# Performance work log

Hardware: AMD Instinct MI355X
Metric: run time of the kernel (lower is better)

## Reference

```python
import jax, jax.numpy as jnp
import numpy as np

IN_DIM = 512
HID = 256
SAMPLE = 8
TAU = 0.5
LAMBDA = 1.0
NUM_MLP = 3


def l2norm(x, axis=-1, eps=1e-12):
    n = jnp.sqrt(jnp.sum(x * x, axis=axis, keepdims=True))
    return x / jnp.maximum(n, eps)


def graphconv(adj, x, W, b):
    # GraphConv: aggregate then linear transform
    return adj @ (x @ W) + b


def mlp(x, Ws, bs):
    h = x
    for i in range(len(Ws) - 1):
        h = jax.nn.relu(h @ Ws[i] + bs[i])
    return h @ Ws[-1] + bs[-1]


def setup_inputs() -> dict:
    key = jax.random.key(0)
    ks = jax.random.split(key, 24)
    N = 16384
    # sparse-ish row-normalized adjacency surrogate (dense storage)
    a1 = jax.random.uniform(ks[0], (N, N), jnp.float32)
    a1 = (a1 > 0.999).astype(jnp.float32)
    adj1 = a1 / jnp.maximum(a1.sum(1, keepdims=True), 1.0)
    a2 = jax.random.uniform(ks[1], (N, N), jnp.float32)
    a2 = (a2 > 0.999).astype(jnp.float32)
    adj2 = a2 / jnp.maximum(a2.sum(1, keepdims=True), 1.0)
    x1 = jax.random.normal(ks[2], (N, IN_DIM), jnp.float32)
    x2 = jax.random.normal(ks[3], (N, IN_DIM), jnp.float32)
    neighbor_idx = jax.random.randint(ks[4], (N, SAMPLE), 0, N)
    neg_idx = jax.random.randint(ks[5], (N, SAMPLE), 0, N)

    def lin(k, fi, fo):
        k1, k2 = jax.random.split(k)
        s = 1.0 / np.sqrt(fi)
        return (jax.random.uniform(k1, (fi, fo), jnp.float32, -s, s),
                jax.random.uniform(k2, (fo,), jnp.float32, -s, s))

    W1, b1 = lin(ks[6], IN_DIM, HID)
    W2, b2 = lin(ks[7], HID, HID)
    tW1, tb1 = lin(ks[8], IN_DIM, HID)
    tW2, tb2 = lin(ks[9], HID, HID)
    projW, projB, semW, semB = [], [], [], []
    for i in range(NUM_MLP):
        w, b = lin(ks[10 + i], HID, HID)
        projW.append(w); projB.append(b)
        w, b = lin(ks[14 + i], HID, HID)
        semW.append(w); semB.append(b)
    return dict(adj1=adj1, adj2=adj2, x1=x1, x2=x2,
                neighbor_idx=neighbor_idx, neg_idx=neg_idx,
                W1=W1, b1=b1, W2=W2, b2=b2,
                tW1=tW1, tb1=tb1, tW2=tW2, tb2=tb2,
                projW0=projW[0], projB0=projB[0], projW1=projW[1], projB1=projB[1], projW2=projW[2], projB2=projB[2],
                semW0=semW[0], semB0=semB[0], semW1=semW[1], semB1=semB[1], semW2=semW[2], semB2=semB[2])


def contrastive_loss(projected_emd, v_emd, samp_u, samp_neg_v):
    # projected_emd, v_emd: [N,1,D]; samp_u, samp_neg_v: [N,S,D]
    pos = jnp.exp(jnp.einsum('nod,nsd->ns', projected_emd, samp_u) / TAU)  # [N,S]
    neg_sum = jnp.sum(jnp.exp(jnp.einsum('nod,nsd->ns', v_emd, samp_neg_v) / TAU), axis=1)  # [N]
    neg_score = jnp.sum(jnp.log(pos + neg_sum[:, None]), axis=1)  # [N]
    pos_score = jnp.sum(jnp.log(pos), axis=1)
    total = jnp.sum(LAMBDA * neg_score - pos_score)
    return total / samp_u.shape[0] / samp_u.shape[1]


def semi_loss(z1, z2):
    z1n = l2norm(z1); z2n = l2norm(z2)
    refl = jnp.exp((z1n @ z1n.T) / TAU)      # [N,N]
    between = jnp.exp((z1n @ z2n.T) / TAU)   # [N,N]
    return -jnp.log(jnp.diagonal(between) / (refl.sum(1) + between.sum(1) - jnp.diagonal(refl)))


def reference(adj1, adj2, x1, x2, neighbor_idx, neg_idx,
              W1, b1, W2, b2, tW1, tb1, tW2, tb2,
              projW0, projB0, projW1, projB1, projW2, projB2,
              semW0, semB0, semW1, semB1, semW2, semB2):
    pW = [projW0, projW1, projW2]; pB = [projB0, projB1, projB2]
    sW = [semW0, semW1, semW2]; sB = [semB0, semB1, semB2]
    h1 = graphconv(adj1, x1, W1, b1)
    h2 = graphconv(adj1, x2, W1, b1)
    h3 = graphconv(adj2, graphconv(adj2, x1, W1, b1), W2, b2)  # v_emd
    u_emd = l2norm(graphconv(adj2, graphconv(adj2, x1, tW1, tb1), tW2, tb2))
    projected = l2norm(mlp(h3, pW, pB))
    h1_proj = l2norm(mlp(h1, sW, sB))
    h2_proj = l2norm(mlp(h2, sW, sB))

    v_norm = l2norm(h3)
    samp_u = u_emd[neighbor_idx]          # [N,S,D]
    samp_neg_v = v_norm[neg_idx]          # [N,S,D]
    gacl = contrastive_loss(projected[:, None, :], v_norm[:, None, :], samp_u, samp_neg_v)

    l1 = semi_loss(h1_proj, h2_proj)
    l2 = semi_loss(h2_proj, h1_proj)
    sem = jnp.mean((l1 + l2) * 0.5)

    total = gacl + 0.6 * sem
    return total, gacl, sem, h3
```

## Files before the change

### kernel.cpp

```cpp
#include <hip/hip_runtime.h>
#include <hip/hip_bf16.h>

#define NN   16384
#define IND  512
#define HID  256
#define SAMP 8
#define CAP  64

typedef __bf16 bf16;
typedef __bf16 bf16x4 __attribute__((ext_vector_type(4)));
typedef __bf16 bf16x8 __attribute__((ext_vector_type(8)));
typedef float  f32x4  __attribute__((ext_vector_type(4)));

#define LOG2E_2 2.8853900817779268f

#define GLOAD_LDS16(gptr, lptr) \
  __builtin_amdgcn_global_load_lds((const __attribute__((address_space(1))) void*)(gptr), \
                                   (__attribute__((address_space(3))) void*)(lptr), 16, 0, 0)

__global__ void cvt_x(const float* __restrict__ a, bf16* __restrict__ oa,
                      const float* __restrict__ b, bf16* __restrict__ ob) {
  const float* src = blockIdx.y ? b : a;
  bf16* dst = blockIdx.y ? ob : oa;
  int stride = gridDim.x * blockDim.x;
  for (int i = blockIdx.x * blockDim.x + threadIdx.x; i < (NN * IND) / 4; i += stride) {
    float4 v = ((const float4*)src)[i];
    bf16x4 o = {(bf16)v.x, (bf16)v.y, (bf16)v.z, (bf16)v.w};
    *(bf16x4*)(dst + (size_t)i * 4) = o;
  }
}

struct WtArgs {
  const float* src[10];
  bf16* dst[10];
  int K[10];
};

__global__ void cvt_weights(WtArgs a) {
  int w = blockIdx.y;
  int K = a.K[w];
  int total = K * HID;
  const float* s = a.src[w];
  bf16* d = a.dst[w];
  for (int i = blockIdx.x * blockDim.x + threadIdx.x; i < total; i += gridDim.x * blockDim.x) {
    int k = i >> 8, n = i & 255;
    d[n * K + k] = (bf16)s[i];
  }
}

__global__ void scan_adj(const float* __restrict__ adjA, const float* __restrict__ adjB,
                         int* __restrict__ colsA, int* __restrict__ cntA,
                         int* __restrict__ colsB, int* __restrict__ cntB) {
  const float* adj = blockIdx.y ? adjB : adjA;
  int* cols = blockIdx.y ? colsB : colsA;
  int* cnt = blockIdx.y ? cntB : cntA;
  int r = blockIdx.x;
  __shared__ int c;
  if (threadIdx.x == 0) c = 0;
  __syncthreads();
  const float4* row = (const float4*)(adj + (size_t)r * NN);
  int* rc = cols + (size_t)r * CAP;
  #pragma unroll 4
  for (int i = threadIdx.x; i < NN / 4; i += 256) {
    float4 v = row[i];
    if (v.x != 0.f || v.y != 0.f || v.z != 0.f || v.w != 0.f) {
      if (v.x != 0.f) { int p = atomicAdd(&c, 1); if (p < CAP) rc[p] = 4 * i; }
      if (v.y != 0.f) { int p = atomicAdd(&c, 1); if (p < CAP) rc[p] = 4 * i + 1; }
      if (v.z != 0.f) { int p = atomicAdd(&c, 1); if (p < CAP) rc[p] = 4 * i + 2; }
      if (v.w != 0.f) { int p = atomicAdd(&c, 1); if (p < CAP) rc[p] = 4 * i + 3; }
    }
  }
  __syncthreads();
  if (threadIdx.x == 0) cnt[r] = (c < CAP) ? c : CAP;
}

struct SpmmB {
  const int* cols[4]; const int* cnt[4]; const float* X[4]; const float* bias[4];
  float* outF[4];
  bf16* outB[4];
  float* outNF[4];
};
__global__ void spmm_b(SpmmB s) {
  int j = blockIdx.y;
  int wid = threadIdx.x >> 6, lane = threadIdx.x & 63;
  int r = blockIdx.x * 4 + wid;
  int c = s.cnt[j][r];
  float val = 1.0f / (float)(c > 0 ? c : 1);
  const int* rc = s.cols[j] + (size_t)r * CAP;
  const float* X = s.X[j];
  float ax = 0.f, ay = 0.f, az = 0.f, aw = 0.f;
  for (int t = 0; t < c; ++t) {
    int col = rc[t];
    float4 v = ((const float4*)(X + (size_t)col * HID))[lane];
    ax += v.x; ay += v.y; az += v.z; aw += v.w;
  }
  float4 b4 = ((const float4*)s.bias[j])[lane];
  ax = ax * val + b4.x; ay = ay * val + b4.y; az = az * val + b4.z; aw = aw * val + b4.w;
  if (s.outF[j]) {
    float* o = s.outF[j] + (size_t)r * HID + lane * 4;
    o[0] = ax; o[1] = ay; o[2] = az; o[3] = aw;
  }
  if (s.outB[j]) {
    bf16x4 ob = {(bf16)ax, (bf16)ay, (bf16)az, (bf16)aw};
    *(bf16x4*)(s.outB[j] + (size_t)r * HID + lane * 4) = ob;
  }
  if (s.outNF[j]) {
    float ss = ax * ax + ay * ay + az * az + aw * aw;
    #pragma unroll
    for (int off = 1; off < 64; off <<= 1) ss += __shfl_xor(ss, off);
    float inv = 1.0f / fmaxf(sqrtf(ss), 1e-12f);
    float4 o = {ax * inv, ay * inv, az * inv, aw * inv};
    ((float4*)(s.outNF[j] + (size_t)r * HID))[lane] = o;
  }
}

struct GemmB {
  const bf16* A[3]; const bf16* Bt[3]; const float* bias[3];
  float* Cf[3]; bf16* Cb[3];
};
__global__ __launch_bounds__(256) void gemm_b(GemmB g, int K, int relu) {
  __shared__ bf16 As[128][64];
  __shared__ bf16 Bs[128][64];
  int j = blockIdx.z;
  const bf16* A = g.A[j];
  const bf16* Bt = g.Bt[j];
  int m0 = blockIdx.x * 128, n0 = blockIdx.y * 128;
  int tid = threadIdx.x, wid = tid >> 6, lane = tid & 63;
  int wm = wid >> 1, wn = wid & 1, q = lane >> 4, li = lane & 15;
  int r8 = lane >> 3, cc8 = lane & 7;
  int csw = cc8 ^ r8;
  f32x4 acc[4][4] = {};
  for (int k0 = 0; k0 < K; k0 += 64) {
    if (k0) __syncthreads();
    const bf16* gA = A + (size_t)(m0 + wid * 32 + r8) * K + k0 + csw * 8;
    const bf16* gB = Bt + (size_t)(n0 + wid * 32 + r8) * K + k0 + csw * 8;
    #pragma unroll
    for (int jj = 0; jj < 4; ++jj) {
      GLOAD_LDS16(gA + (size_t)jj * 8 * K, &As[wid * 32 + jj * 8][0]);
      GLOAD_LDS16(gB + (size_t)jj * 8 * K, &Bs[wid * 32 + jj * 8][0]);
    }
    __syncthreads();
    #pragma unroll
    for (int kk = 0; kk < 64; kk += 32) {
      int ca = (((q + (kk >> 3)) ^ (li & 7)) << 3);
      bf16x8 af[4], bfr[4];
      #pragma unroll
      for (int im = 0; im < 4; ++im) af[im] = *(const bf16x8*)(&As[wm * 64 + im * 16 + li][ca]);
      #pragma unroll
      for (int in = 0; in < 4; ++in) bfr[in] = *(const bf16x8*)(&Bs[wn * 64 + in * 16 + li][ca]);
      #pragma unroll
      for (int im = 0; im < 4; ++im)
        #pragma unroll
        for (int in = 0; in < 4; ++in)
          acc[im][in] = __builtin_amdgcn_mfma_f32_16x16x32_bf16(af[im], bfr[in], acc[im][in], 0, 0, 0);
    }
  }
  float* Cf = g.Cf[j];
  bf16* Cb = g.Cb[j];
  const float* bias = g.bias[j];
  #pragma unroll
  for (int im = 0; im < 4; ++im) {
    int grow0 = m0 + wm * 64 + im * 16 + q * 4;
    #pragma unroll
    for (int in = 0; in < 4; ++in) {
      int gcol = n0 + wn * 64 + in * 16 + li;
      float bv = bias ? bias[gcol] : 0.f;
      #pragma unroll
      for (int reg = 0; reg < 4; ++reg) {
        float v = acc[im][in][reg] + bv;
        if (relu) v = fmaxf(v, 0.f);
        size_t idx = (size_t)(grow0 + reg) * HID + gcol;
        if (Cf) Cf[idx] = v;
        if (Cb) Cb[idx] = (bf16)v;
      }
    }
  }
}

__global__ __launch_bounds__(256) void flash_sem2(
    const bf16* __restrict__ P, const bf16* __restrict__ Q,
    float* __restrict__ Ra, float* __restrict__ Rb,
    float* __restrict__ Cr, float* __restrict__ Cc) {
  __shared__ bf16 As[128][64];
  __shared__ bf16 Bs[128][64];
  int z = blockIdx.z;
  int bid = blockIdx.y * 128 + blockIdx.x;
  int grp = bid >> 8, loc = bid & 255;
  int bx = (grp & 7) * 16 + (loc & 15);
  int by = (grp >> 3) * 16 + (loc >> 4);
  if (z < 2 && by < bx) return;
  const bf16* X = (z == 1) ? Q : P;
  const bf16* Y = (z == 0) ? P : Q;
  float* rowacc = (z == 0) ? Ra : (z == 1) ? Rb : Cr;
  float* colacc = (z == 2) ? Cc : rowacc;
  bool docol = (z == 2) || (bx != by);
  int m0 = bx * 128, n0 = by * 128;
  int tid = threadIdx.x, wid = tid >> 6, lane = tid & 63;
  int wm = wid >> 1, wn = wid & 1, q = lane >> 4, li = lane & 15;
  int r8 = lane >> 3, cc8 = lane & 7;
  int csw = cc8 ^ r8;
  f32x4 acc[4][4] = {};
  for (int k0 = 0; k0 < HID; k0 += 64) {
    if (k0) __syncthreads();
    const bf16* gA = X + (size_t)(m0 + wid * 32 + r8) * HID + k0 + csw * 8;
    const bf16* gB = Y + (size_t)(n0 + wid * 32 + r8) * HID + k0 + csw * 8;
    #pragma unroll
    for (int jj = 0; jj < 4; ++jj) {
      GLOAD_LDS16(gA + (size_t)jj * 8 * HID, &As[wid * 32 + jj * 8][0]);
      GLOAD_LDS16(gB + (size_t)jj * 8 * HID, &Bs[wid * 32 + jj * 8][0]);
    }
    __syncthreads();
    #pragma unroll
    for (int kk = 0; kk < 64; kk += 32) {
      int ca = (((q + (kk >> 3)) ^ (li & 7)) << 3);
      bf16x8 af[4], bfr[4];
      #pragma unroll
      for (int im = 0; im < 4; ++im) af[im] = *(const bf16x8*)(&As[wm * 64 + im * 16 + li][ca]);
      #pragma unroll
      for (int in = 0; in < 4; ++in) bfr[in] = *(const bf16x8*)(&Bs[wn * 64 + in * 16 + li][ca]);
      #pragma unroll
      for (int im = 0; im < 4; ++im)
        #pragma unroll
        for (int in = 0; in < 4; ++in)
          acc[im][in] = __builtin_amdgcn_mfma_f32_16x16x32_bf16(af[im], bfr[in], acc[im][in], 0, 0, 0);
    }
  }
  float cs[4] = {0.f, 0.f, 0.f, 0.f};
  #pragma unroll
  for (int im = 0; im < 4; ++im) {
    #pragma unroll
    for (int reg = 0; reg < 4; ++reg) {
      float rs = 0.f;
      #pragma unroll
      for (int in = 0; in < 4; ++in) {
        float e = exp2f(acc[im][in][reg] * LOG2E_2);
        rs += e;
        cs[in] += e;
      }
      rs += __shfl_xor(rs, 1); rs += __shfl_xor(rs, 2);
      rs += __shfl_xor(rs, 4); rs += __shfl_xor(rs, 8);
      if (li == 0) atomicAdd(&rowacc[m0 + wm * 64 + im * 16 + q * 4 + reg], rs);
    }
  }
  if (docol) {
    #pragma unroll
    for (int in = 0; in < 4; ++in) {
      float v = cs[in];
      v += __shfl_xor(v, 16); v += __shfl_xor(v, 32);
      if (q == 0) atomicAdd(&colacc[n0 + wn * 64 + in * 16 + li], v);
    }
  }
}

struct NormB { const float* X[3]; float* outF[3]; bf16* outB[3]; };
__global__ void l2norm_b(NormB n) {
  int j = blockIdx.y;
  int wid = threadIdx.x >> 6, lane = threadIdx.x & 63;
  int r = blockIdx.x * 4 + wid;
  float4 a = ((const float4*)(n.X[j] + (size_t)r * HID))[lane];
  float s = a.x * a.x + a.y * a.y + a.z * a.z + a.w * a.w;
  #pragma unroll
  for (int off = 1; off < 64; off <<= 1) s += __shfl_xor(s, off);
  float inv = 1.0f / fmaxf(sqrtf(s), 1e-12f);
  a.x *= inv; a.y *= inv; a.z *= inv; a.w *= inv;
  if (n.outF[j]) ((float4*)(n.outF[j] + (size_t)r * HID))[lane] = a;
  if (n.outB[j]) {
    bf16x4 b = {(bf16)a.x, (bf16)a.y, (bf16)a.z, (bf16)a.w};
    *(bf16x4*)(n.outB[j] + (size_t)r * HID + lane * 4) = b;
  }
}

__global__ void contrast_k(const float* __restrict__ proj, const float* __restrict__ vn,
                           const float* __restrict__ ue, const int* __restrict__ nbr,
                           const int* __restrict__ neg, float* __restrict__ gsum) {
  int wid = threadIdx.x >> 6, lane = threadIdx.x & 63;
  int n = blockIdx.x * 4 + wid;
  float4 p = ((const float4*)(proj + (size_t)n * HID))[lane];
  float4 v = ((const float4*)(vn + (size_t)n * HID))[lane];
  float du[SAMP], dn[SAMP];
  for (int s = 0; s < SAMP; ++s) {
    int iu = nbr[n * SAMP + s];
    float4 u = ((const float4*)(ue + (size_t)iu * HID))[lane];
    float d = p.x * u.x + p.y * u.y + p.z * u.z + p.w * u.w;
    #pragma unroll
    for (int off = 1; off < 64; off <<= 1) d += __shfl_xor(d, off);
    du[s] = d;
    int iv = neg[n * SAMP + s];
    float4 w = ((const float4*)(vn + (size_t)iv * HID))[lane];
    float d2 = v.x * w.x + v.y * w.y + v.z * w.z + v.w * w.w;
    #pragma unroll
    for (int off = 1; off < 64; off <<= 1) d2 += __shfl_xor(d2, off);
    dn[s] = d2;
  }
  float negsum = 0.f;
  for (int s = 0; s < SAMP; ++s) negsum += expf(2.f * dn[s]);
  float ns = 0.f, ps = 0.f;
  for (int s = 0; s < SAMP; ++s) {
    float pl = 2.f * du[s];
    ns += logf(expf(pl) + negsum);
    ps += pl;
  }
  if (lane == 0) atomicAdd(gsum, ns - ps);
}

__global__ void sem_fin(const float* __restrict__ P, const float* __restrict__ Q2,
                        const float* __restrict__ Ra, const float* __restrict__ Rb,
                        const float* __restrict__ Cr, const float* __restrict__ Cc,
                        float* __restrict__ ssum) {
  int wid = threadIdx.x >> 6, lane = threadIdx.x & 63;
  int i = blockIdx.x * 4 + wid;
  float4 a = ((const float4*)(P + (size_t)i * HID))[lane];
  float4 b = ((const float4*)(Q2 + (size_t)i * HID))[lane];
  float d = a.x * b.x + a.y * b.y + a.z * b.z + a.w * b.w;
  #pragma unroll
  for (int off = 1; off < 64; off <<= 1) d += __shfl_xor(d, off);
  float db = expf(2.f * d);
  float e2 = expf(2.f);
  float l1 = -logf(db / (Ra[i] + Cr[i] - e2));
  float l2 = -logf(db / (Rb[i] + Cc[i] - e2));
  if (lane == 0) atomicAdd(ssum, 0.5f * (l1 + l2));
}

__global__ void final_k(const float* __restrict__ sums, float* __restrict__ out) {
  float gacl = sums[0] / (float)(NN * SAMP);
  float sem = sums[1] / (float)NN;
  out[0] = gacl + 0.6f * sem;
  out[1] = gacl;
  out[2] = sem;
}

extern "C" void kernel_launch(void* const* d_in, const int* in_sizes, int n_in,
                              void* d_out, int out_size, void* d_ws, size_t ws_size,
                              hipStream_t stream) {
  (void)in_sizes; (void)n_in; (void)out_size; (void)ws_size;
  const float* adj1 = (const float*)d_in[0];
  const float* adj2 = (const float*)d_in[1];
  const float* x1 = (const float*)d_in[2];
  const float* x2 = (const float*)d_in[3];
  const int* nbr = (const int*)d_in[4];
  const int* neg = (const int*)d_in[5];
  const float* W1 = (const float*)d_in[6];
  const float* b1 = (const float*)d_in[7];
  const float* W2 = (const float*)d_in[8];
  const float* b2 = (const float*)d_in[9];
  const float* tW1 = (const float*)d_in[10];
  const float* tb1 = (const float*)d_in[11];
  const float* tW2 = (const float*)d_in[12];
  const float* tb2 = (const float*)d_in[13];
  const float* pB[3] = {(const float*)d_in[15], (const float*)d_in[17], (const float*)d_in[19]};
  const float* sB[3] = {(const float*)d_in[21], (const float*)d_in[23], (const float*)d_in[25]};

  char* w = (char*)d_ws;
  auto alloc = [&](size_t bytes) -> char* {
    char* p = w;
    w += (bytes + 255) & ~(size_t)255;
    return p;
  };
  float* Ra = (float*)alloc((size_t)NN * 4);
  float* Rb = (float*)alloc((size_t)NN * 4);
  float* Cr = (float*)alloc((size_t)NN * 4);
  float* Cc = (float*)alloc((size_t)NN * 4);
  float* sums = (float*)alloc(256);
  size_t accBytes = (size_t)(w - (char*)d_ws);

  int* c1cols = (int*)alloc((size_t)NN * CAP * 4);
  int* c1cnt = (int*)alloc((size_t)NN * 4);
  int* c2cols = (int*)alloc((size_t)NN * CAP * 4);
  int* c2cnt = (int*)alloc((size_t)NN * 4);
  bf16* x1b = (bf16*)alloc((size_t)NN * IND * 2);
  bf16* x2b = (bf16*)alloc((size_t)NN * IND * 2);
  bf16* W1t = (bf16*)alloc((size_t)IND * HID * 2);
  bf16* tW1t = (bf16*)alloc((size_t)IND * HID * 2);
  bf16* W2t = (bf16*)alloc((size_t)HID * HID * 2);
  bf16* tW2t = (bf16*)alloc((size_t)HID * HID * 2);
  bf16* pWt[3], *sWt[3];
  for (int i = 0; i < 3; ++i) pWt[i] = (bf16*)alloc((size_t)HID * HID * 2);
  for (int i = 0; i < 3; ++i) sWt[i] = (bf16*)alloc((size_t)HID * HID * 2);
  const size_t FB = (size_t)NN * HID * 4;
  float* xw1 = (float*)alloc(FB);
  float* xw2 = (float*)alloc(FB);
  float* xt1 = (float*)alloc(FB);
  float* mlp_out = (float*)alloc(FB);
  float* projected = (float*)alloc(FB);
  float* h1p = (float*)alloc(FB);
  float* h2p = (float*)alloc(FB);
  float* v_norm = (float*)alloc(FB);
  float* gw = xw2;
  float* utw = xt1;
  float* u_emd = xw1;
  const size_t BB = (size_t)NN * HID * 2;
  bf16* h1b = (bf16*)alloc(BB);
  bf16* h2b = (bf16*)alloc(BB);
  bf16* gb = (bf16*)alloc(BB);
  bf16* h3b = (bf16*)alloc(BB);
  bf16* utb = (bf16*)alloc(BB);
  bf16* mA = (bf16*)alloc(BB);
  bf16* mB = (bf16*)alloc(BB);
  bf16* mB1 = x1b;
  bf16* mB2 = x1b + (size_t)NN * HID;
  bf16* Pb = gb;
  bf16* Qb = utb;

  hipMemsetAsync(d_ws, 0, accBytes, stream);

  WtArgs wa;
  const float* wsrc[10] = {W1, tW1, W2, tW2,
                           (const float*)d_in[14], (const float*)d_in[16], (const float*)d_in[18],
                           (const float*)d_in[20], (const float*)d_in[22], (const float*)d_in[24]};
  bf16* wdst[10] = {W1t, tW1t, W2t, tW2t, pWt[0], pWt[1], pWt[2], sWt[0], sWt[1], sWt[2]};
  int wk[10] = {IND, IND, HID, HID, HID, HID, HID, HID, HID, HID};
  for (int i = 0; i < 10; ++i) { wa.src[i] = wsrc[i]; wa.dst[i] = wdst[i]; wa.K[i] = wk[i]; }
  cvt_weights<<<dim3(512, 10), 256, 0, stream>>>(wa);
  cvt_x<<<dim3(2048, 2), 256, 0, stream>>>(x1, x1b, x2, x2b);
  scan_adj<<<dim3(NN, 2), 256, 0, stream>>>(adj1, adj2, c1cols, c1cnt, c2cols, c2cnt);

  {
    GemmB g = {};
    g.A[0] = x1b; g.Bt[0] = W1t; g.Cf[0] = xw1;
    g.A[1] = x2b; g.Bt[1] = W1t; g.Cf[1] = xw2;
    g.A[2] = x1b; g.Bt[2] = tW1t; g.Cf[2] = xt1;
    gemm_b<<<dim3(128, 2, 3), 256, 0, stream>>>(g, IND, 0);
  }
  {
    SpmmB s = {};
    s.cols[0] = c1cols; s.cnt[0] = c1cnt; s.X[0] = xw1; s.bias[0] = b1; s.outB[0] = h1b;
    s.cols[1] = c1cols; s.cnt[1] = c1cnt; s.X[1] = xw2; s.bias[1] = b1; s.outB[1] = h2b;
    s.cols[2] = c2cols; s.cnt[2] = c2cnt; s.X[2] = xw1; s.bias[2] = b1; s.outB[2] = gb;
    s.cols[3] = c2cols; s.cnt[3] = c2cnt; s.X[3] = xt1; s.bias[3] = tb1; s.outB[3] = utb;
    spmm_b<<<dim3(NN / 4, 4), 256, 0, stream>>>(s);
  }
  {
    GemmB g = {};
    g.A[0] = gb; g.Bt[0] = W2t; g.Cf[0] = gw;
    g.A[1] = utb; g.Bt[1] = tW2t; g.Cf[1] = utw;
    gemm_b<<<dim3(128, 2, 2), 256, 0, stream>>>(g, HID, 0);
  }
  float* h3out = ((float*)d_out) + 3;
  {
    SpmmB s = {};
    s.cols[0] = c2cols; s.cnt[0] = c2cnt; s.X[0] = gw; s.bias[0] = b2;
    s.outF[0] = h3out; s.outB[0] = h3b; s.outNF[0] = v_norm;
    s.cols[1] = c2cols; s.cnt[1] = c2cnt; s.X[1] = utw; s.bias[1] = tb2;
    s.outNF[1] = u_emd;
    spmm_b<<<dim3(NN / 4, 2), 256, 0, stream>>>(s);
  }
  {
    GemmB g = {};
    g.A[0] = h3b; g.Bt[0] = pWt[0]; g.bias[0] = pB[0]; g.Cb[0] = mA;
    g.A[1] = h1b; g.Bt[1] = sWt[0]; g.bias[1] = sB[0]; g.Cb[1] = gb;
    g.A[2] = h2b; g.Bt[2] = sWt[0]; g.bias[2] = sB[0]; g.Cb[2] = utb;
    gemm_b<<<dim3(128, 2, 3), 256, 0, stream>>>(g, HID, 1);
  }
  {
    GemmB g = {};
    g.A[0] = mA; g.Bt[0] = pWt[1]; g.bias[0] = pB[1]; g.Cb[0] = mB;
    g.A[1] = gb; g.Bt[1] = sWt[1]; g.bias[1] = sB[1]; g.Cb[1] = mB1;
    g.A[2] = utb; g.Bt[2] = sWt[1]; g.bias[2] = sB[1]; g.Cb[2] = mB2;
    gemm_b<<<dim3(128, 2, 3), 256, 0, stream>>>(g, HID, 1);
  }
  {
    GemmB g = {};
    g.A[0] = mB; g.Bt[0] = pWt[2]; g.bias[0] = pB[2]; g.Cf[0] = mlp_out;
    g.A[1] = mB1; g.Bt[1] = sWt[2]; g.bias[1] = sB[2]; g.Cf[1] = xw2;
    g.A[2] = mB2; g.Bt[2] = sWt[2]; g.bias[2] = sB[2]; g.Cf[2] = xt1;
    gemm_b<<<dim3(128, 2, 3), 256, 0, stream>>>(g, HID, 0);
  }
  {
    NormB nb2 = {};
    nb2.X[0] = mlp_out; nb2.outF[0] = projected;
    nb2.X[1] = xw2; nb2.outF[1] = h1p; nb2.outB[1] = Pb;
    nb2.X[2] = xt1; nb2.outF[2] = h2p; nb2.outB[2] = Qb;
    l2norm_b<<<dim3(NN / 4, 3), 256, 0, stream>>>(nb2);
  }

  flash_sem2<<<dim3(128, 128, 3), 256, 0, stream>>>(Pb, Qb, Ra, Rb, Cr, Cc);
  contrast_k<<<NN / 4, 256, 0, stream>>>(projected, v_norm, u_emd, nbr, neg, &sums[0]);
  sem_fin<<<NN / 4, 256, 0, stream>>>(h1p, h2p, Ra, Rb, Cr, Cc, &sums[1]);
  final_k<<<1, 1, 0, stream>>>(sums, (float*)d_out);
}
```

Before: 3.420 ms.

## Drop LDS staging in similarity kernel and merge tail reduction kernels

The all-pairs exp-similarity kernel now runs 2 waves per block, each owning a 64x128 sub-tile, and reads its bf16 MFMA operands directly from global memory instead of staging them through swizzled shared memory. This removes the LDS traffic and barriers, relying on L2/L1 caching of the 128-row blocks instead, and doubles accumulator registers per wave. The contrastive and semantic finalization kernels are merged into one launch split by blockIdx.y to save a launch. The risk is more global/L1 traffic and register pressure, which may reduce occupancy.

```diff
diff --git a/kernel.cpp b/kernel.cpp
--- a/kernel.cpp
+++ b/kernel.cpp
@@ -177,12 +177,10 @@
   }
 }
 
-__global__ __launch_bounds__(256) void flash_sem2(
+__global__ __launch_bounds__(128, 2) void flash_sem3(
     const bf16* __restrict__ P, const bf16* __restrict__ Q,
     float* __restrict__ Ra, float* __restrict__ Rb,
     float* __restrict__ Cr, float* __restrict__ Cc) {
-  __shared__ bf16 As[128][64];
-  __shared__ bf16 Bs[128][64];
   int z = blockIdx.z;
   int bid = blockIdx.y * 128 + blockIdx.x;
   int grp = bid >> 8, loc = bid & 255;
@@ -195,59 +193,49 @@
   float* colacc = (z == 2) ? Cc : rowacc;
   bool docol = (z == 2) || (bx != by);
   int m0 = bx * 128, n0 = by * 128;
-  int tid = threadIdx.x, wid = tid >> 6, lane = tid & 63;
-  int wm = wid >> 1, wn = wid & 1, q = lane >> 4, li = lane & 15;
-  int r8 = lane >> 3, cc8 = lane & 7;
-  int csw = cc8 ^ r8;
-  f32x4 acc[4][4] = {};
-  for (int k0 = 0; k0 < HID; k0 += 64) {
-    if (k0) __syncthreads();
-    const bf16* gA = X + (size_t)(m0 + wid * 32 + r8) * HID + k0 + csw * 8;
-    const bf16* gB = Y + (size_t)(n0 + wid * 32 + r8) * HID + k0 + csw * 8;
-    #pragma unroll
-    for (int jj = 0; jj < 4; ++jj) {
-      GLOAD_LDS16(gA + (size_t)jj * 8 * HID, &As[wid * 32 + jj * 8][0]);
-      GLOAD_LDS16(gB + (size_t)jj * 8 * HID, &Bs[wid * 32 + jj * 8][0]);
-    }
-    __syncthreads();
-    #pragma unroll
-    for (int kk = 0; kk < 64; kk += 32) {
-      int ca = (((q + (kk >> 3)) ^ (li & 7)) << 3);
-      bf16x8 af[4], bfr[4];
-      #pragma unroll
-      for (int im = 0; im < 4; ++im) af[im] = *(const bf16x8*)(&As[wm * 64 + im * 16 + li][ca]);
-      #pragma unroll
-      for (int in = 0; in < 4; ++in) bfr[in] = *(const bf16x8*)(&Bs[wn * 64 + in * 16 + li][ca]);
-      #pragma unroll
-      for (int im = 0; im < 4; ++im)
-        #pragma unroll
-        for (int in = 0; in < 4; ++in)
-          acc[im][in] = __builtin_amdgcn_mfma_f32_16x16x32_bf16(af[im], bfr[in], acc[im][in], 0, 0, 0);
-    }
-  }
-  float cs[4] = {0.f, 0.f, 0.f, 0.f};
+  int wid = threadIdx.x >> 6, lane = threadIdx.x & 63;
+  int q = lane >> 4, li = lane & 15;
+  const bf16* Arow = X + (size_t)(m0 + wid * 64 + li) * HID + q * 8;
+  const bf16* Brow = Y + (size_t)(n0 + li) * HID + q * 8;
+  f32x4 acc[4][8] = {};
+  #pragma unroll
+  for (int kk = 0; kk < 8; ++kk) {
+    bf16x8 af[4], bfr[8];
+    #pragma unroll
+    for (int im = 0; im < 4; ++im)
+      af[im] = *(const bf16x8*)(Arow + (size_t)im * 16 * HID + kk * 32);
+    #pragma unroll
+    for (int in = 0; in < 8; ++in)
+      bfr[in] = *(const bf16x8*)(Brow + (size_t)in * 16 * HID + kk * 32);
+    #pragma unroll
+    for (int im = 0; im < 4; ++im)
+      #pragma unroll
+      for (int in = 0; in < 8; ++in)
+        acc[im][in] = __builtin_amdgcn_mfma_f32_16x16x32_bf16(af[im], bfr[in], acc[im][in], 0, 0, 0);
+  }
+  float cs[8] = {};
   #pragma unroll
   for (int im = 0; im < 4; ++im) {
     #pragma unroll
     for (int reg = 0; reg < 4; ++reg) {
       float rs = 0.f;
       #pragma unroll
-      for (int in = 0; in < 4; ++in) {
+      for (int in = 0; in < 8; ++in) {
         float e = exp2f(acc[im][in][reg] * LOG2E_2);
         rs += e;
         cs[in] += e;
       }
       rs += __shfl_xor(rs, 1); rs += __shfl_xor(rs, 2);
       rs += __shfl_xor(rs, 4); rs += __shfl_xor(rs, 8);
-      if (li == 0) atomicAdd(&rowacc[m0 + wm * 64 + im * 16 + q * 4 + reg], rs);
+      if (li == 0) atomicAdd(&rowacc[m0 + wid * 64 + im * 16 + q * 4 + reg], rs);
     }
   }
   if (docol) {
     #pragma unroll
-    for (int in = 0; in < 4; ++in) {
+    for (int in = 0; in < 8; ++in) {
       float v = cs[in];
       v += __shfl_xor(v, 16); v += __shfl_xor(v, 32);
-      if (q == 0) atomicAdd(&colacc[n0 + wn * 64 + in * 16 + li], v);
+      if (q == 0) atomicAdd(&colacc[n0 + in * 16 + li], v);
     }
   }
 }
@@ -270,55 +258,54 @@
   }
 }
 
-__global__ void contrast_k(const float* __restrict__ proj, const float* __restrict__ vn,
-                           const float* __restrict__ ue, const int* __restrict__ nbr,
-                           const int* __restrict__ neg, float* __restrict__ gsum) {
+__global__ void tail_k(const float* __restrict__ proj, const float* __restrict__ vn,
+                       const float* __restrict__ ue, const int* __restrict__ nbr,
+                       const int* __restrict__ neg,
+                       const float* __restrict__ P, const float* __restrict__ Q2,
+                       const float* __restrict__ Ra, const float* __restrict__ Rb,
+                       const float* __restrict__ Cr, const float* __restrict__ Cc,
+                       float* __restrict__ sums) {
   int wid = threadIdx.x >> 6, lane = threadIdx.x & 63;
   int n = blockIdx.x * 4 + wid;
-  float4 p = ((const float4*)(proj + (size_t)n * HID))[lane];
-  float4 v = ((const float4*)(vn + (size_t)n * HID))[lane];
-  float du[SAMP], dn[SAMP];
-  for (int s = 0; s < SAMP; ++s) {
-    int iu = nbr[n * SAMP + s];
-    float4 u = ((const float4*)(ue + (size_t)iu * HID))[lane];
-    float d = p.x * u.x + p.y * u.y + p.z * u.z + p.w * u.w;
+  if (blockIdx.y == 0) {
+    float4 p = ((const float4*)(proj + (size_t)n * HID))[lane];
+    float4 v = ((const float4*)(vn + (size_t)n * HID))[lane];
+    float du[SAMP], dn[SAMP];
+    for (int s = 0; s < SAMP; ++s) {
+      int iu = nbr[n * SAMP + s];
+      float4 u = ((const float4*)(ue + (size_t)iu * HID))[lane];
+      float d = p.x * u.x + p.y * u.y + p.z * u.z + p.w * u.w;
+      #pragma unroll
+      for (int off = 1; off < 64; off <<= 1) d += __shfl_xor(d, off);
+      du[s] = d;
+      int iv = neg[n * SAMP + s];
+      float4 w = ((const float4*)(vn + (size_t)iv * HID))[lane];
+      float d2 = v.x * w.x + v.y * w.y + v.z * w.z + v.w * w.w;
+      #pragma unroll
+      for (int off = 1; off < 64; off <<= 1) d2 += __shfl_xor(d2, off);
+      dn[s] = d2;
+    }
+    float negsum = 0.f;
+    for (int s = 0; s < SAMP; ++s) negsum += expf(2.f * dn[s]);
+    float ns = 0.f, ps = 0.f;
+    for (int s = 0; s < SAMP; ++s) {
+      float pl = 2.f * du[s];
+      ns += logf(expf(pl) + negsum);
+      ps += pl;
+    }
+    if (lane == 0) atomicAdd(&sums[0], ns - ps);
+  } else {
+    float4 a = ((const float4*)(P + (size_t)n * HID))[lane];
+    float4 b = ((const float4*)(Q2 + (size_t)n * HID))[lane];
+    float d = a.x * b.x + a.y * b.y + a.z * b.z + a.w * b.w;
     #pragma unroll
     for (int off = 1; off < 64; off <<= 1) d += __shfl_xor(d, off);
-    du[s] = d;
-    int iv = neg[n * SAMP + s];
-    float4 w = ((const float4*)(vn + (size_t)iv * HID))[lane];
-    float d2 = v.x * w.x + v.y * w.y + v.z * w.z + v.w * w.w;
-    #pragma unroll
-    for (int off = 1; off < 64; off <<= 1) d2 += __shfl_xor(d2, off);
-    dn[s] = d2;
-  }
-  float negsum = 0.f;
-  for (int s = 0; s < SAMP; ++s) negsum += expf(2.f * dn[s]);
-  float ns = 0.f, ps = 0.f;
-  for (int s = 0; s < SAMP; ++s) {
-    float pl = 2.f * du[s];
-    ns += logf(expf(pl) + negsum);
-    ps += pl;
-  }
-  if (lane == 0) atomicAdd(gsum, ns - ps);
-}
-
-__global__ void sem_fin(const float* __restrict__ P, const float* __restrict__ Q2,
-                        const float* __restrict__ Ra, const float* __restrict__ Rb,
-                        const float* __restrict__ Cr, const float* __restrict__ Cc,
-                        float* __restrict__ ssum) {
-  int wid = threadIdx.x >> 6, lane = threadIdx.x & 63;
-  int i = blockIdx.x * 4 + wid;
-  float4 a = ((const float4*)(P + (size_t)i * HID))[lane];
-  float4 b = ((const float4*)(Q2 + (size_t)i * HID))[lane];
-  float d = a.x * b.x + a.y * b.y + a.z * b.z + a.w * b.w;
-  #pragma unroll
-  for (int off = 1; off < 64; off <<= 1) d += __shfl_xor(d, off);
-  float db = expf(2.f * d);
-  float e2 = expf(2.f);
-  float l1 = -logf(db / (Ra[i] + Cr[i] - e2));
-  float l2 = -logf(db / (Rb[i] + Cc[i] - e2));
-  if (lane == 0) atomicAdd(ssum, 0.5f * (l1 + l2));
+    float db = expf(2.f * d);
+    float e2 = expf(2.f);
+    float l1 = -logf(db / (Ra[n] + Cr[n] - e2));
+    float l2 = -logf(db / (Rb[n] + Cc[n] - e2));
+    if (lane == 0) atomicAdd(&sums[1], 0.5f * (l1 + l2));
+  }
 }
 
 __global__ void final_k(const float* __restrict__ sums, float* __restrict__ out) {
@@ -473,8 +460,8 @@
     l2norm_b<<<dim3(NN / 4, 3), 256, 0, stream>>>(nb2);
   }
 
-  flash_sem2<<<dim3(128, 128, 3), 256, 0, stream>>>(Pb, Qb, Ra, Rb, Cr, Cc);
-  contrast_k<<<NN / 4, 256, 0, stream>>>(projected, v_norm, u_emd, nbr, neg, &sums[0]);
-  sem_fin<<<NN / 4, 256, 0, stream>>>(h1p, h2p, Ra, Rb, Cr, Cc, &sums[1]);
+  flash_sem3<<<dim3(128, 128, 3), 128, 0, stream>>>(Pb, Qb, Ra, Rb, Cr, Cc);
+  tail_k<<<dim3(NN / 4, 2), 256, 0, stream>>>(projected, v_norm, u_emd, nbr, neg,
+                                              h1p, h2p, Ra, Rb, Cr, Cc, sums);
   final_k<<<1, 1, 0, stream>>>(sums, (float*)d_out);
 }
```

After: 3.614 ms. 1.06x slower.
